# Kernel tuning notes

Hardware: AMD Instinct MI355X
Metric: run time of the kernel (lower is better)

Reference implementation:

```python
import jax, jax.numpy as jnp
import numpy as np

B, S, E, H = 2, 2048, 1024, 16
D = E // H  # head_dim = 64


def setup_inputs() -> dict:
    key = jax.random.key(0)
    ks = jax.random.split(key, 8)
    s = 0.02
    return {
        "queries": jax.random.normal(ks[0], (B, S, E), jnp.float32),
        "keys": jax.random.normal(ks[1], (B, S, E), jnp.float32),
        "values": jax.random.normal(ks[2], (B, S, E), jnp.float32),
        "mask": jnp.ones((B, 1, 1, S), jnp.int32),
        "Wq": jax.random.normal(ks[3], (E, E), jnp.float32) * s,
        "bq": jnp.zeros((E,), jnp.float32),
        "Wk": jax.random.normal(ks[4], (E, E), jnp.float32) * s,
        "bk": jnp.zeros((E,), jnp.float32),
        "Wv": jax.random.normal(ks[5], (E, E), jnp.float32) * s,
        "bv": jnp.zeros((E,), jnp.float32),
        "Wo": jax.random.normal(ks[6], (E, E), jnp.float32) * s,
        "bo": jnp.zeros((E,), jnp.float32),
    }


def reference(queries, keys, values, mask, Wq, bq, Wk, bk, Wv, bv, Wo, bo):
    # NOTE: faithful to source, W_v is applied to the `keys` input; `values` is unused.
    q = queries @ Wq.T + bq            # [B,S,E]
    k = keys @ Wk.T + bk               # [B,S,E]
    v = keys @ Wv.T + bv               # [B,S,E]
    q = q.reshape(B, S, H, D)
    k = k.reshape(B, S, H, D)
    v = v.reshape(B, S, H, D)
    scale = 1.0 / jnp.sqrt(jnp.asarray(D, q.dtype))
    scores = jnp.einsum("nqhd,nkhd->nhqk", q, k)   # [B,H,S,S] full score matrix
    scores = jnp.where(mask == 0, jnp.asarray(-1e20, scores.dtype), scores)
    attn = jax.nn.softmax(scores * scale, axis=-1)
    out = jnp.einsum("nhqk,nkhd->nqhd", attn, v).reshape(B, S, E)
    return out @ Wo.T + bo
```

## Files before the change

kernel.cpp:

```cpp
#include <hip/hip_runtime.h>
#include <hip/hip_bf16.h>
#include <stdint.h>

#define NB 2
#define NS 2048
#define NE 1024
#define NH 16
#define ND 64
#define NTS 16

typedef __attribute__((ext_vector_type(4))) float f32x4;
typedef __attribute__((ext_vector_type(16))) float f32x16;
typedef __attribute__((ext_vector_type(8))) short s16x8;
typedef __attribute__((ext_vector_type(4))) unsigned short u16x4;
typedef __attribute__((ext_vector_type(2))) unsigned int uint2v;

__device__ __forceinline__ unsigned short f2bf(float f) {
  union { float f; unsigned int i; } u; u.f = f;
  unsigned int r = u.i + 0x7FFFu + ((u.i >> 16) & 1u);
  return (unsigned short)(r >> 16);
}
__device__ __forceinline__ float bf2f(unsigned short u) {
  union { unsigned int i; float f; } x; x.i = ((unsigned int)u) << 16; return x.f;
}

__device__ __forceinline__ unsigned cvtpk_bf16(float lo, float hi) {
  unsigned r;
  asm("v_cvt_pk_bf16_f32 %0, %1, %2" : "=v"(r) : "v"(lo), "v"(hi));
  return r;
}

__device__ __forceinline__ void gload_lds16(const void* g, void* l) {
  __builtin_amdgcn_global_load_lds(
      (const __attribute__((address_space(1))) uint32_t*)g,
      (__attribute__((address_space(3))) uint32_t*)l, 16, 0, 0);
}

__device__ __forceinline__ f32x4 mfma16(s16x8 a, s16x8 b, f32x4 c) {
  return __builtin_amdgcn_mfma_f32_16x16x32_bf16(a, b, c, 0, 0, 0);
}
__device__ __forceinline__ f32x16 mfma32(s16x8 a, s16x8 b, f32x16 c) {
  return __builtin_amdgcn_mfma_f32_32x32x16_bf16(a, b, c, 0, 0, 0);
}

__global__ void conv_x2(const float* __restrict__ a, const float* __restrict__ b,
                        unsigned short* __restrict__ da, unsigned short* __restrict__ db,
                        int n4) {
  const float* s = blockIdx.y ? b : a;
  unsigned short* d = blockIdx.y ? db : da;
  int i = blockIdx.x * blockDim.x + threadIdx.x;
  int stride = gridDim.x * blockDim.x;
  for (; i < n4; i += stride) {
    float4 v = ((const float4*)s)[i];
    u16x4 o;
    o.x = f2bf(v.x); o.y = f2bf(v.y); o.z = f2bf(v.z); o.w = f2bf(v.w);
    ((u16x4*)d)[i] = o;
  }
}

__global__ void conv_w4(const float* __restrict__ s0, const float* __restrict__ s1,
                        const float* __restrict__ s2, const float* __restrict__ s3,
                        unsigned short* __restrict__ d0, unsigned short* __restrict__ d1,
                        unsigned short* __restrict__ d2, unsigned short* __restrict__ d3,
                        int n4) {
  const float* s; unsigned short* d;
  switch (blockIdx.y) {
    case 0: s = s0; d = d0; break;
    case 1: s = s1; d = d1; break;
    case 2: s = s2; d = d2; break;
    default: s = s3; d = d3; break;
  }
  int i = blockIdx.x * blockDim.x + threadIdx.x;
  int stride = gridDim.x * blockDim.x;
  for (; i < n4; i += stride) {
    float4 v = ((const float4*)s)[i];
    u16x4 o;
    o.x = f2bf(v.x); o.y = f2bf(v.y); o.z = f2bf(v.z); o.w = f2bf(v.w);
    ((u16x4*)d)[i] = o;
  }
}

__global__ void mask_pack(const int* __restrict__ mask, unsigned long long* __restrict__ bm) {
  int w = blockIdx.x;
  int lane = threadIdx.x;
  int mk = mask[w * 64 + lane];
  unsigned long long bal = __ballot(mk != 0);
  if (lane == 0) bm[w] = bal;
}

__global__ __launch_bounds__(256, 3) void gemm_qkv(
    const unsigned short* __restrict__ Aq, const unsigned short* __restrict__ Akv,
    const unsigned short* __restrict__ Wqp, const unsigned short* __restrict__ Wkp,
    const unsigned short* __restrict__ Wvp,
    const float* __restrict__ bqp, const float* __restrict__ bkp, const float* __restrict__ bvp,
    unsigned short* __restrict__ outq, unsigned short* __restrict__ outk,
    unsigned short* __restrict__ outvt) {
  constexpr int BM = 64, K = 1024;
  __shared__ char smem[2 * (BM * 128 + 16384)];
  const int t = threadIdx.x;
  const int lane = t & 63;
  const int wv = t >> 6;
  const int wr = wv >> 1, wc = wv & 1;
  const int x = blockIdx.x;
  const int bm = blockIdx.y * BM;
  const int lr = lane & 15, lg = lane >> 4;

  const unsigned short* A; const unsigned short* Wp; const float* bp;
  unsigned short* outp; int nloc, mode;
  float qsc;
  if (x < 8)       { A = Aq;  Wp = Wqp; bp = bqp; outp = outq;  nloc = x * 128;        mode = 0; qsc = 0.18033688f; }
  else if (x < 16) { A = Akv; Wp = Wkp; bp = bkp; outp = outk;  nloc = (x - 8) * 128;  mode = 0; qsc = 1.0f; }
  else             { A = Akv; Wp = Wvp; bp = bvp; outp = outvt; nloc = (x - 16) * 128; mode = 1; qsc = 1.0f; }

  f32x4 acc[2][4] = {};

  auto stage = [&](int buf, int k0) {
    char* As = smem + buf * (BM * 128 + 16384);
    char* Bs = As + BM * 128;
#pragma unroll
    for (int r = 0; r < 2; ++r) {
      int lin = r * 256 + t;
      int row = lin >> 3;
      int scb = ((lin & 7) << 4) ^ ((row & 7) << 4);
      gload_lds16((const char*)(A + (size_t)(bm + row) * K + k0) + scb,
                  As + (size_t)(r * 256 + (t & ~63)) * 16);
    }
#pragma unroll
    for (int r = 0; r < 4; ++r) {
      int lin = r * 256 + t;
      int row = lin >> 3;
      int scb = ((lin & 7) << 4) ^ ((row & 7) << 4);
      gload_lds16((const char*)(Wp + (size_t)(nloc + row) * K + k0) + scb,
                  Bs + (size_t)(r * 256 + (t & ~63)) * 16);
    }
  };

  stage(0, 0);
  for (int t6 = 0; t6 < K / 64; ++t6) {
    const int cur = t6 & 1;
    if (t6 + 1 < K / 64) {
      stage(cur ^ 1, (t6 + 1) * 64);
      asm volatile("s_waitcnt vmcnt(6)" ::: "memory");
    } else {
      asm volatile("s_waitcnt vmcnt(0)" ::: "memory");
    }
    asm volatile("s_barrier" ::: "memory");

    const char* As = smem + cur * (BM * 128 + 16384);
    const char* Bs = As + BM * 128;
    s16x8 af[2][2], bfr[4][2];
#pragma unroll
    for (int mf = 0; mf < 2; ++mf)
#pragma unroll
      for (int kk = 0; kk < 2; ++kk) {
        int row = wr * 32 + mf * 16 + lr;
        int cb = (lg << 4) + (kk << 6);
        af[mf][kk] = *(const s16x8*)(As + row * 128 + (cb ^ ((row & 7) << 4)));
      }
#pragma unroll
    for (int nf = 0; nf < 4; ++nf)
#pragma unroll
      for (int kk = 0; kk < 2; ++kk) {
        int row = wc * 64 + nf * 16 + lr;
        int cb = (lg << 4) + (kk << 6);
        bfr[nf][kk] = *(const s16x8*)(Bs + row * 128 + (cb ^ ((row & 7) << 4)));
      }
#pragma unroll
    for (int mf = 0; mf < 2; ++mf)
#pragma unroll
      for (int nf = 0; nf < 4; ++nf)
#pragma unroll
        for (int kk = 0; kk < 2; ++kk)
          acc[mf][nf] = mfma16(af[mf][kk], bfr[nf][kk], acc[mf][nf]);

    asm volatile("s_waitcnt lgkmcnt(0)" ::: "memory");
    asm volatile("s_barrier" ::: "memory");
  }

#pragma unroll
  for (int mf = 0; mf < 2; ++mf)
#pragma unroll
    for (int nf = 0; nf < 4; ++nf) {
      int m0 = bm + wr * 32 + mf * 16 + (lg << 2);
      int nc = wc * 64 + nf * 16 + lr;
      float bv = bp[nloc + nc];
      if (mode == 0) {
#pragma unroll
        for (int r = 0; r < 4; ++r)
          outp[(size_t)(m0 + r) * 1024 + nloc + nc] = f2bf((acc[mf][nf][r] + bv) * qsc);
      } else {
        int b = m0 >> 11, s = m0 & 2047;
        u16x4 o;
        o.x = f2bf(acc[mf][nf][0] + bv);
        o.y = f2bf(acc[mf][nf][1] + bv);
        o.z = f2bf(acc[mf][nf][2] + bv);
        o.w = f2bf(acc[mf][nf][3] + bv);
        *(u16x4*)&outp[((size_t)b * NE + nloc + nc) * NS + s] = o;
      }
    }
}

__global__ __launch_bounds__(256, 3) void gemm_o(
    const unsigned short* __restrict__ A, const unsigned short* __restrict__ W,
    const float* __restrict__ bias, float* __restrict__ out) {
  constexpr int BM = 64, K = 1024;
  __shared__ char smem[2 * (BM * 128 + 16384)];
  const int t = threadIdx.x;
  const int lane = t & 63;
  const int wv = t >> 6;
  const int wr = wv >> 1, wc = wv & 1;
  const int bm = blockIdx.y * BM, bn = blockIdx.x * 128;
  const int lr = lane & 15, lg = lane >> 4;

  f32x4 acc[2][4] = {};

  auto stage = [&](int buf, int k0) {
    char* As = smem + buf * (BM * 128 + 16384);
    char* Bs = As + BM * 128;
#pragma unroll
    for (int r = 0; r < 2; ++r) {
      int lin = r * 256 + t;
      int row = lin >> 3;
      int scb = ((lin & 7) << 4) ^ ((row & 7) << 4);
      gload_lds16((const char*)(A + (size_t)(bm + row) * K + k0) + scb,
                  As + (size_t)(r * 256 + (t & ~63)) * 16);
    }
#pragma unroll
    for (int r = 0; r < 4; ++r) {
      int lin = r * 256 + t;
      int row = lin >> 3;
      int scb = ((lin & 7) << 4) ^ ((row & 7) << 4);
      gload_lds16((const char*)(W + (size_t)(bn + row) * K + k0) + scb,
                  Bs + (size_t)(r * 256 + (t & ~63)) * 16);
    }
  };

  stage(0, 0);
  for (int t6 = 0; t6 < K / 64; ++t6) {
    const int cur = t6 & 1;
    if (t6 + 1 < K / 64) {
      stage(cur ^ 1, (t6 + 1) * 64);
      asm volatile("s_waitcnt vmcnt(6)" ::: "memory");
    } else {
      asm volatile("s_waitcnt vmcnt(0)" ::: "memory");
    }
    asm volatile("s_barrier" ::: "memory");

    const char* As = smem + cur * (BM * 128 + 16384);
    const char* Bs = As + BM * 128;
    s16x8 af[2][2], bfr[4][2];
#pragma unroll
    for (int mf = 0; mf < 2; ++mf)
#pragma unroll
      for (int kk = 0; kk < 2; ++kk) {
        int row = wr * 32 + mf * 16 + lr;
        int cb = (lg << 4) + (kk << 6);
        af[mf][kk] = *(const s16x8*)(As + row * 128 + (cb ^ ((row & 7) << 4)));
      }
#pragma unroll
    for (int nf = 0; nf < 4; ++nf)
#pragma unroll
      for (int kk = 0; kk < 2; ++kk) {
        int row = wc * 64 + nf * 16 + lr;
        int cb = (lg << 4) + (kk << 6);
        bfr[nf][kk] = *(const s16x8*)(Bs + row * 128 + (cb ^ ((row & 7) << 4)));
      }
#pragma unroll
    for (int mf = 0; mf < 2; ++mf)
#pragma unroll
      for (int nf = 0; nf < 4; ++nf)
#pragma unroll
        for (int kk = 0; kk < 2; ++kk)
          acc[mf][nf] = mfma16(af[mf][kk], bfr[nf][kk], acc[mf][nf]);

    asm volatile("s_waitcnt lgkmcnt(0)" ::: "memory");
    asm volatile("s_barrier" ::: "memory");
  }

#pragma unroll
  for (int mf = 0; mf < 2; ++mf)
#pragma unroll
    for (int nf = 0; nf < 4; ++nf) {
      int m0 = bm + wr * 32 + mf * 16 + (lg << 2);
      int n = bn + wc * 64 + nf * 16 + lr;
      float bv = bias[n];
#pragma unroll
      for (int r = 0; r < 4; ++r)
        out[(size_t)(m0 + r) * 1024 + n] = acc[mf][nf][r] + bv;
    }
}

__global__ __launch_bounds__(256, 2) void attn_fwd(
    const unsigned short* __restrict__ qb, const unsigned short* __restrict__ kb,
    const unsigned short* __restrict__ vt, const unsigned long long* __restrict__ bmw,
    unsigned short* __restrict__ op0, unsigned short* __restrict__ op1,
    float* __restrict__ lp) {
  __shared__ char smem[40960];
  const int t = threadIdx.x, lane = t & 63, wv = t >> 6;
  const int l31 = lane & 31, hi = lane >> 5;
  const int sw = (l31 & 15) << 4;
  const int bh = blockIdx.y, b = bh >> 4, h = bh & 15;
  const int sp = blockIdx.z;
  const int kbase = sp * 1024;
  const int q = blockIdx.x * 128 + wv * 32 + l31;
  unsigned short* opp = sp ? op1 : op0;

  s16x8 qf[4];
#pragma unroll
  for (int ks = 0; ks < 4; ++ks)
    qf[ks] = *(const s16x8*)&qb[((size_t)(b * NS + q)) * NE + h * ND + ks * 16 + hi * 8];

  unsigned long long mword = bmw[(size_t)b * 32 + l31];
  unsigned mlo = (unsigned)mword, mhi = (unsigned)(mword >> 32);

  const char* kSrc[2]; const char* vSrc[2]; int ldsO[2];
#pragma unroll
  for (int r = 0; r < 2; ++r) {
    int L = (r * 256 + t) * 16;
    int row = L >> 8;
    int offp = (L & 255) ^ ((row & 15) << 4);
    int rr = row + ((offp >> 7) << 5);
    int byo = offp & 127;
    kSrc[r] = (const char*)&kb[((size_t)(b * NS + kbase) + rr) * NE + h * ND] + byo;
    vSrc[r] = (const char*)&vt[((size_t)((b * NH + h) * ND) + rr) * NS + kbase] + byo;
    ldsO[r] = (r * 256 + (t & ~63)) * 16;
  }

  int off16[8];
#pragma unroll
  for (int j = 0; j < 8; ++j)
    off16[j] = l31 * 256 + ((j * 32 + hi * 16) ^ sw);

  auto stage = [&](int j) {
    char* kb_ = smem + (j & 1) * 8192;
    char* vb_ = smem + 16384 + (j % 3) * 8192;
#pragma unroll
    for (int r = 0; r < 2; ++r)
      gload_lds16(kSrc[r] + (size_t)j * (64 * NE * 2), kb_ + ldsO[r]);
#pragma unroll
    for (int r = 0; r < 2; ++r)
      gload_lds16(vSrc[r] + (size_t)j * (64 * 2), vb_ + ldsO[r]);
  };

  f32x16 oacc[2] = {};
  f32x16 lacc = {};
  s16x8 pfp[4];

  auto qk = [&](const char* Ks, f32x16& st0, f32x16& st1) {
#pragma unroll
    for (int ks = 0; ks < 4; ++ks) {
      s16x8 kf = *(const s16x8*)(Ks + off16[ks]);
      st0 = mfma32(kf, qf[ks], st0);
    }
#pragma unroll
    for (int ks = 0; ks < 4; ++ks) {
      s16x8 kf = *(const s16x8*)(Ks + off16[4 + ks]);
      st1 = mfma32(kf, qf[ks], st1);
    }
  };

  auto pv = [&](const char* Vs) {
#pragma unroll
    for (int td = 0; td < 2; ++td)
#pragma unroll
      for (int ks = 0; ks < 4; ++ks) {
        s16x8 vf = *(const s16x8*)(Vs + off16[td * 4 + ks]);
        oacc[td] = mfma32(vf, pfp[ks], oacc[td]);
      }
  };

  auto smpack = [&](int tt, f32x16& st0, f32x16& st1) {
#pragma unroll
    for (int r = 0; r < 16; ++r) st0[r] = __builtin_amdgcn_exp2f(st0[r] - 6.0f);
#pragma unroll
    for (int r = 0; r < 16; ++r) st1[r] = __builtin_amdgcn_exp2f(st1[r] - 6.0f);

    int g = sp * NTS + tt;
    unsigned lo = (unsigned)__builtin_amdgcn_readlane((int)mlo, g);
    unsigned hh = (unsigned)__builtin_amdgcn_readlane((int)mhi, g);
    unsigned long long bal = ((unsigned long long)hh << 32) | lo;
    if (bal != ~0ull) {
#pragma unroll
      for (int r = 0; r < 16; ++r) {
        int key0 = (r & 3) + 8 * (r >> 2) + 4 * hi;
        if (!((bal >> key0) & 1)) st0[r] = 0.f;
        if (!((bal >> (key0 + 32)) & 1)) st1[r] = 0.f;
      }
    }

    lacc += st0;
    lacc += st1;

#pragma unroll
    for (int ks = 0; ks < 4; ++ks) {
      const int r0 = (ks & 1) * 8;
      unsigned wreg[4];
#pragma unroll
      for (int w = 0; w < 2; ++w) {
        float e0, e1, e2, e3;
        if (ks < 2) {
          e0 = st0[r0 + 2 * w]; e1 = st0[r0 + 2 * w + 1];
          e2 = st0[r0 + 4 + 2 * w]; e3 = st0[r0 + 4 + 2 * w + 1];
        } else {
          e0 = st1[r0 + 2 * w]; e1 = st1[r0 + 2 * w + 1];
          e2 = st1[r0 + 4 + 2 * w]; e3 = st1[r0 + 4 + 2 * w + 1];
        }
        unsigned x = cvtpk_bf16(e0, e1);
        unsigned y = cvtpk_bf16(e2, e3);
        uint2v r2 = __builtin_amdgcn_permlane32_swap(x, y, false, false);
        wreg[w] = r2.x;
        wreg[w + 2] = r2.y;
      }
      union { unsigned u[4]; s16x8 v; } pu;
      pu.u[0] = wreg[0]; pu.u[1] = wreg[1]; pu.u[2] = wreg[2]; pu.u[3] = wreg[3];
      pfp[ks] = pu.v;
    }
  };

  stage(0);
  asm volatile("s_waitcnt vmcnt(0)" ::: "memory");
  __builtin_amdgcn_s_barrier();
  stage(1);
  {
    f32x16 s0 = {}, s1 = {};
    __builtin_amdgcn_s_setprio(1);
    qk(smem, s0, s1);
    __builtin_amdgcn_s_setprio(0);
    smpack(0, s0, s1);
  }

#pragma unroll 1
  for (int tt = 1; tt < NTS; ++tt) {
    asm volatile("s_waitcnt vmcnt(0)" ::: "memory");
    __builtin_amdgcn_s_barrier();
    if (tt + 1 < NTS) stage(tt + 1);

    const char* Kb = smem + (tt & 1) * 8192;
    const char* Vb = smem + 16384 + ((tt - 1) % 3) * 8192;
    f32x16 s0 = {}, s1 = {};
    __builtin_amdgcn_s_setprio(1);
    qk(Kb, s0, s1);
    pv(Vb);
    __builtin_amdgcn_s_setprio(0);
    smpack(tt, s0, s1);
  }

  __builtin_amdgcn_s_setprio(1);
  pv(smem + 16384 + ((NTS - 1) % 3) * 8192);
  __builtin_amdgcn_s_setprio(0);

  float l0 = 0.f;
#pragma unroll
  for (int r = 0; r < 16; ++r) l0 += lacc[r];
  float l = l0 + __shfl_xor(l0, 32);
  if (hi == 0) lp[(((size_t)sp * NB + b) * NH + h) * NS + q] = l;

  __syncthreads();
  char* Ob = smem + wv * 4096;
#pragma unroll
  for (int td = 0; td < 2; ++td)
#pragma unroll
    for (int i = 0; i < 8; ++i) {
      int r = 2 * i;
      int d = td * 32 + (r & 3) + 8 * (r >> 2) + 4 * hi;
      unsigned pk = cvtpk_bf16(oacc[td][r], oacc[td][r + 1]);
      *(unsigned*)(Ob + l31 * 128 + ((d * 2) ^ ((l31 & 7) << 4))) = pk;
    }
#pragma unroll
  for (int p4 = 0; p4 < 4; ++p4) {
    int lq = p4 * 8 + (lane >> 3);
    int col = (lane & 7) * 16;
    s16x8 v0 = *(const s16x8*)(Ob + lq * 128 + (col ^ ((lq & 7) << 4)));
    int qg = blockIdx.x * 128 + wv * 32 + lq;
    *(s16x8*)((char*)&opp[((size_t)(b * NS + qg)) * NE + h * ND] + col) = v0;
  }
}

__global__ void attn_combine(const unsigned short* __restrict__ o0,
                             const unsigned short* __restrict__ o1,
                             const float* __restrict__ lp,
                             unsigned short* __restrict__ ao) {
  int idx = blockIdx.x * 256 + threadIdx.x;
  size_t f = (size_t)idx * 8;
  int b = (int)(f >> 21);
  int s = (int)((f >> 10) & 2047);
  int h = (int)((f >> 6) & 15);
  float l0 = lp[((size_t)(b * NH + h)) * NS + s];
  float l1 = lp[(size_t)NB * NH * NS + ((size_t)(b * NH + h)) * NS + s];
  float inv = 1.0f / (l0 + l1);
  s16x8 a0 = ((const s16x8*)o0)[idx];
  s16x8 a1 = ((const s16x8*)o1)[idx];
  u16x4 r0, r1;
#pragma unroll
  for (int j = 0; j < 4; ++j) {
    float v = (bf2f((unsigned short)a0[j]) + bf2f((unsigned short)a1[j])) * inv;
    ((unsigned short*)&r0)[j] = f2bf(v);
  }
#pragma unroll
  for (int j = 0; j < 4; ++j) {
    float v = (bf2f((unsigned short)a0[4 + j]) + bf2f((unsigned short)a1[4 + j])) * inv;
    ((unsigned short*)&r1)[j] = f2bf(v);
  }
  ((u16x4*)ao)[idx * 2] = r0;
  ((u16x4*)ao)[idx * 2 + 1] = r1;
}

extern "C" void kernel_launch(void* const* d_in, const int* in_sizes, int n_in,
                              void* d_out, int out_size, void* d_ws, size_t ws_size,
                              hipStream_t stream) {
  const float* queries = (const float*)d_in[0];
  const float* keys = (const float*)d_in[1];
  const int* mask = (const int*)d_in[3];
  const float* Wq = (const float*)d_in[4];
  const float* bq = (const float*)d_in[5];
  const float* Wk = (const float*)d_in[6];
  const float* bk = (const float*)d_in[7];
  const float* Wv = (const float*)d_in[8];
  const float* bv = (const float*)d_in[9];
  const float* Wo = (const float*)d_in[10];
  const float* bo = (const float*)d_in[11];
  float* out = (float*)d_out;

  char* ws = (char*)d_ws;
  const size_t SZ_X = (size_t)NB * NS * NE * 2;
  const size_t SZ_W = (size_t)NE * NE * 2;
  unsigned short* qbf = (unsigned short*)(ws);
  unsigned short* kbf = (unsigned short*)(ws + SZ_X);
  unsigned short* wqb = (unsigned short*)(ws + 2 * SZ_X);
  unsigned short* wkb = (unsigned short*)(ws + 2 * SZ_X + SZ_W);
  unsigned short* wvb = (unsigned short*)(ws + 2 * SZ_X + 2 * SZ_W);
  unsigned short* wob = (unsigned short*)(ws + 2 * SZ_X + 3 * SZ_W);
  unsigned short* qp  = (unsigned short*)(ws + 2 * SZ_X + 4 * SZ_W);
  unsigned short* kp  = (unsigned short*)(ws + 3 * SZ_X + 4 * SZ_W);
  unsigned short* vtp = (unsigned short*)(ws + 4 * SZ_X + 4 * SZ_W);
  unsigned short* ao  = (unsigned short*)(ws + 5 * SZ_X + 4 * SZ_W);
  unsigned long long* bmp = (unsigned long long*)(ws + 6 * SZ_X + 4 * SZ_W);
  unsigned short* op0 = qbf;
  unsigned short* op1 = kbf;
  float* lpart = (float*)wqb;

  int nX4 = NB * NS * NE / 4, nW4 = NE * NE / 4;
  conv_x2<<<dim3(1024, 2), 256, 0, stream>>>(queries, keys, qbf, kbf, nX4);
  conv_w4<<<dim3(256, 4), 256, 0, stream>>>(Wq, Wk, Wv, Wo, wqb, wkb, wvb, wob, nW4);
  mask_pack<<<NB * NS / 64, 64, 0, stream>>>(mask, bmp);

  gemm_qkv<<<dim3(24, 64), 256, 0, stream>>>(qbf, kbf, wqb, wkb, wvb,
                                             bq, bk, bv, qp, kp, vtp);

  dim3 ga(NS / 128, NB * NH, 2);
  attn_fwd<<<ga, 256, 0, stream>>>(qp, kp, vtp, bmp, op0, op1, lpart);
  attn_combine<<<4096, 256, 0, stream>>>(op0, op1, lpart, ao);

  gemm_o<<<dim3(8, 64), 256, 0, stream>>>(ao, wob, bo, out);
}
```

Before: 123.9 us.

## Fuse prep kernels into one launch and raise attention occupancy

Merges the activation conversion, weight conversion and mask packing kernels into a single prep launch, with block-index ranges selecting the task, to cut launch overhead and gaps between launches. Raises attn_fwd launch bounds from 2 to 3 blocks per CU. Shrinks the row-sum accumulator from 16 to 8 floats by pairwise-adding the score tiles, which frees registers so the higher occupancy target is easier to meet. Tighter register limits may cause spills in the attention kernel.

Result: no change. 123.9 us (+0.0%).

```diff
diff --git a/kernel.cpp b/kernel.cpp
--- a/kernel.cpp
+++ b/kernel.cpp
@@ -10,6 +10,7 @@
 #define NTS 16
 
 typedef __attribute__((ext_vector_type(4))) float f32x4;
+typedef __attribute__((ext_vector_type(8))) float f32x8;
 typedef __attribute__((ext_vector_type(16))) float f32x16;
 typedef __attribute__((ext_vector_type(8))) short s16x8;
 typedef __attribute__((ext_vector_type(4))) unsigned short u16x4;
@@ -43,49 +44,49 @@
   return __builtin_amdgcn_mfma_f32_32x32x16_bf16(a, b, c, 0, 0, 0);
 }
 
-__global__ void conv_x2(const float* __restrict__ a, const float* __restrict__ b,
-                        unsigned short* __restrict__ da, unsigned short* __restrict__ db,
-                        int n4) {
-  const float* s = blockIdx.y ? b : a;
-  unsigned short* d = blockIdx.y ? db : da;
-  int i = blockIdx.x * blockDim.x + threadIdx.x;
-  int stride = gridDim.x * blockDim.x;
-  for (; i < n4; i += stride) {
-    float4 v = ((const float4*)s)[i];
-    u16x4 o;
-    o.x = f2bf(v.x); o.y = f2bf(v.y); o.z = f2bf(v.z); o.w = f2bf(v.w);
-    ((u16x4*)d)[i] = o;
-  }
-}
-
-__global__ void conv_w4(const float* __restrict__ s0, const float* __restrict__ s1,
-                        const float* __restrict__ s2, const float* __restrict__ s3,
-                        unsigned short* __restrict__ d0, unsigned short* __restrict__ d1,
-                        unsigned short* __restrict__ d2, unsigned short* __restrict__ d3,
-                        int n4) {
-  const float* s; unsigned short* d;
-  switch (blockIdx.y) {
-    case 0: s = s0; d = d0; break;
-    case 1: s = s1; d = d1; break;
-    case 2: s = s2; d = d2; break;
-    default: s = s3; d = d3; break;
-  }
-  int i = blockIdx.x * blockDim.x + threadIdx.x;
-  int stride = gridDim.x * blockDim.x;
-  for (; i < n4; i += stride) {
-    float4 v = ((const float4*)s)[i];
-    u16x4 o;
-    o.x = f2bf(v.x); o.y = f2bf(v.y); o.z = f2bf(v.z); o.w = f2bf(v.w);
-    ((u16x4*)d)[i] = o;
-  }
-}
-
-__global__ void mask_pack(const int* __restrict__ mask, unsigned long long* __restrict__ bm) {
-  int w = blockIdx.x;
-  int lane = threadIdx.x;
-  int mk = mask[w * 64 + lane];
-  unsigned long long bal = __ballot(mk != 0);
-  if (lane == 0) bm[w] = bal;
+__global__ void prep(const float* __restrict__ xq, const float* __restrict__ xk,
+                     unsigned short* __restrict__ dq, unsigned short* __restrict__ dk,
+                     const float* __restrict__ w0, const float* __restrict__ w1,
+                     const float* __restrict__ w2, const float* __restrict__ w3,
+                     unsigned short* __restrict__ e0, unsigned short* __restrict__ e1,
+                     unsigned short* __restrict__ e2, unsigned short* __restrict__ e3,
+                     const int* __restrict__ mask, unsigned long long* __restrict__ bm) {
+  const int bid = blockIdx.x, t = threadIdx.x;
+  if (bid < 2048) {
+    const float* s = (bid < 1024) ? xq : xk;
+    unsigned short* d = (bid < 1024) ? dq : dk;
+    int i = (bid & 1023) * 256 + t;
+    const int n4 = NB * NS * NE / 4, stride = 1024 * 256;
+    for (; i < n4; i += stride) {
+      float4 v = ((const float4*)s)[i];
+      u16x4 o;
+      o.x = f2bf(v.x); o.y = f2bf(v.y); o.z = f2bf(v.z); o.w = f2bf(v.w);
+      ((u16x4*)d)[i] = o;
+    }
+  } else if (bid < 3072) {
+    int seg = (bid - 2048) >> 8;
+    const float* s; unsigned short* d;
+    switch (seg) {
+      case 0: s = w0; d = e0; break;
+      case 1: s = w1; d = e1; break;
+      case 2: s = w2; d = e2; break;
+      default: s = w3; d = e3; break;
+    }
+    int i = ((bid - 2048) & 255) * 256 + t;
+    const int n4 = NE * NE / 4, stride = 256 * 256;
+    for (; i < n4; i += stride) {
+      float4 v = ((const float4*)s)[i];
+      u16x4 o;
+      o.x = f2bf(v.x); o.y = f2bf(v.y); o.z = f2bf(v.z); o.w = f2bf(v.w);
+      ((u16x4*)d)[i] = o;
+    }
+  } else {
+    int w = (bid - 3072) * 4 + (t >> 6);
+    int lane = t & 63;
+    int mk = mask[w * 64 + lane];
+    unsigned long long bal = __ballot(mk != 0);
+    if (lane == 0) bm[w] = bal;
+  }
 }
 
 __global__ __launch_bounds__(256, 3) void gemm_qkv(
@@ -290,7 +291,7 @@
     }
 }
 
-__global__ __launch_bounds__(256, 2) void attn_fwd(
+__global__ __launch_bounds__(256, 3) void attn_fwd(
     const unsigned short* __restrict__ qb, const unsigned short* __restrict__ kb,
     const unsigned short* __restrict__ vt, const unsigned long long* __restrict__ bmw,
     unsigned short* __restrict__ op0, unsigned short* __restrict__ op1,
@@ -343,7 +344,7 @@
   };
 
   f32x16 oacc[2] = {};
-  f32x16 lacc = {};
+  f32x8 lacc = {};
   s16x8 pfp[4];
 
   auto qk = [&](const char* Ks, f32x16& st0, f32x16& st1) {
@@ -388,8 +389,9 @@
       }
     }
 
-    lacc += st0;
-    lacc += st1;
+#pragma unroll
+    for (int r = 0; r < 8; ++r)
+      lacc[r] += (st0[r] + st1[r]) + (st0[r + 8] + st1[r + 8]);
 
 #pragma unroll
     for (int ks = 0; ks < 4; ++ks) {
@@ -451,7 +453,7 @@
 
   float l0 = 0.f;
 #pragma unroll
-  for (int r = 0; r < 16; ++r) l0 += lacc[r];
+  for (int r = 0; r < 8; ++r) l0 += lacc[r];
   float l = l0 + __shfl_xor(l0, 32);
   if (hi == 0) lp[(((size_t)sp * NB + b) * NH + h) * NS + q] = l;
 
@@ -539,10 +541,9 @@
   unsigned short* op1 = kbf;
   float* lpart = (float*)wqb;
 
-  int nX4 = NB * NS * NE / 4, nW4 = NE * NE / 4;
-  conv_x2<<<dim3(1024, 2), 256, 0, stream>>>(queries, keys, qbf, kbf, nX4);
-  conv_w4<<<dim3(256, 4), 256, 0, stream>>>(Wq, Wk, Wv, Wo, wqb, wkb, wvb, wob, nW4);
-  mask_pack<<<NB * NS / 64, 64, 0, stream>>>(mask, bmp);
+  prep<<<3088, 256, 0, stream>>>(queries, keys, qbf, kbf,
+                                 Wq, Wk, Wv, Wo, wqb, wkb, wvb, wob,
+                                 mask, bmp);
 
   gemm_qkv<<<dim3(24, 64), 256, 0, stream>>>(qbf, kbf, wqb, wkb, wvb,
                                              bq, bk, bv, qp, kp, vtp);
```
